# Kernel optimization log

Hardware: AMD Instinct MI355X
Metric: run time of the kernel (lower is better)

The kernel has to match this reference:

```python
import jax, jax.numpy as jnp
import numpy as np

D_MODEL = 1024
NUM_HEADS = 16
D_K = D_MODEL // NUM_HEADS
NEG = -1000000000.0


def setup_inputs() -> dict:
    key = jax.random.key(0)
    ks = jax.random.split(key, 9)
    B, S, D = 2, 2048, D_MODEL
    scale = 1.0 / np.sqrt(D)
    return {
        "query": jax.random.normal(ks[0], (B, S, D), jnp.float32),
        "key": jax.random.normal(ks[1], (B, S, D), jnp.float32),
        "value": jax.random.normal(ks[2], (B, S, D), jnp.float32),
        "mask": jax.random.randint(ks[3], (B, S, S), 0, 2, jnp.int32),
        # torch nn.Linear stores weight as (out_features, in_features); y = x @ W.T
        "W_q": jax.random.normal(ks[4], (D, D), jnp.float32) * scale,
        "W_k": jax.random.normal(ks[5], (D, D), jnp.float32) * scale,
        "W_v": jax.random.normal(ks[6], (D, D), jnp.float32) * scale,
        "W_o": jax.random.normal(ks[7], (D, D), jnp.float32) * scale,
        "b_o": jax.random.normal(ks[8], (D,), jnp.float32) * 0.01,
    }


def reference(query, key, value, mask, W_q, W_k, W_v, W_o, b_o):
    B, S, D = query.shape
    H, dk = NUM_HEADS, D_K
    # projections (torch Linear: x @ W.T), then split heads -> [B, H, S, dk]
    def split_heads(x, W):
        return jnp.einsum('bsd,ed->bse', x, W).reshape(B, S, H, dk).transpose(0, 2, 1, 3)
    Q = split_heads(query, W_q)
    K = split_heads(key, W_k)
    V = split_heads(value, W_v)
    scores = jnp.einsum('bhqd,bhkd->bhqk', Q, K) / jnp.sqrt(jnp.float32(dk))
    scores = jnp.where(mask[:, None, :, :] == 0, NEG, scores)
    attn = jax.nn.softmax(scores, axis=-1)  # dropout inactive in eval mode
    out = jnp.einsum('bhqk,bhkd->bhqd', attn, V)  # [B, H, S, dk]
    out = out.transpose(0, 2, 1, 3).reshape(B, S, D)
    return jnp.einsum('bsd,ed->bse', out, W_o) + b_o
```

## Files before the change

### kernel.cpp

```cpp
#include <hip/hip_runtime.h>
#include <hip/hip_bf16.h>
#include <stdint.h>

typedef __attribute__((ext_vector_type(4))) float f32x4;
typedef __attribute__((ext_vector_type(8))) short bf16x8;
typedef __attribute__((ext_vector_type(4))) unsigned short us4;
typedef unsigned short ushort_t;
typedef unsigned long long u64;

#define LOG2E 1.44269504088896340f
#define NEGB  -1.0e9f

__device__ __forceinline__ unsigned short f2bf(float x){
  union { float f; uint32_t u; } v; v.f = x;
  uint32_t u = v.u + 0x7fffu + ((v.u >> 16) & 1u);
  return (unsigned short)(u >> 16);
}

__device__ __forceinline__ void gld16(const void* g, void* l){
  __builtin_amdgcn_global_load_lds(
      (const __attribute__((address_space(1))) unsigned int*)g,
      (__attribute__((address_space(3))) unsigned int*)l, 16, 0, 0);
}

__global__ void prep_all(const float4* __restrict__ q, const float4* __restrict__ k,
                         const float4* __restrict__ v, const float4* __restrict__ wq,
                         const float4* __restrict__ wk, const float4* __restrict__ wv,
                         const float4* __restrict__ wo, ushort_t* __restrict__ dst,
                         const int4* __restrict__ mask, u64* __restrict__ mb){
  int bid = blockIdx.x;
  if (bid < 16384){
    int i = bid * 256 + threadIdx.x;
    const float4* src; int base;
    if      (i < 1048576){ src = q;  base = 0; }
    else if (i < 2097152){ src = k;  base = 1048576; }
    else if (i < 3145728){ src = v;  base = 2097152; }
    else if (i < 3407872){ src = wq; base = 3145728; }
    else if (i < 3670016){ src = wk; base = 3407872; }
    else if (i < 3932160){ src = wv; base = 3670016; }
    else                 { src = wo; base = 3932160; }
    float4 f = src[i - base];
    us4 o; o.x = f2bf(f.x); o.y = f2bf(f.y); o.z = f2bf(f.z); o.w = f2bf(f.w);
    ((us4*)dst)[i] = o;
  } else {
    int w = (bid - 16384) * 256 + threadIdx.x;
    const int4* p = mask + (size_t)w * 16;
    u64 bits = 0;
    #pragma unroll
    for (int j = 0; j < 16; j++){
      int4 m = p[j];
      bits |= (u64)(m.x != 0) << (j*4);
      bits |= (u64)(m.y != 0) << (j*4+1);
      bits |= (u64)(m.z != 0) << (j*4+2);
      bits |= (u64)(m.w != 0) << (j*4+3);
    }
    mb[w] = bits;
  }
}

__global__ void gemm_qkv(const ushort_t* __restrict__ qb, const ushort_t* __restrict__ kb,
                         const ushort_t* __restrict__ vb, const ushort_t* __restrict__ wqb,
                         const ushort_t* __restrict__ wkb, const ushort_t* __restrict__ wvb,
                         ushort_t* __restrict__ Qh, ushort_t* __restrict__ Kh,
                         ushort_t* __restrict__ Vt, float qscale){
  __shared__ ushort_t As[2][4096];
  __shared__ ushort_t Bs[2][4096];
  const int z = blockIdx.z;
  const ushort_t* A = (z == 0) ? qb  : (z == 1) ? kb  : vb;
  const ushort_t* B = (z == 0) ? wqb : (z == 1) ? wkb : wvb;
  ushort_t*       C = (z == 0) ? Qh  : (z == 1) ? Kh  : Vt;
  const float scale = (z == 0) ? qscale : 1.0f;

  const int tid = threadIdx.x, wave = tid >> 6, lane = tid & 63;
  const int m0 = blockIdx.x * 128, n0 = blockIdx.y * 128;
  const int wr = wave >> 1, wc = wave & 1;
  f32x4 acc[4][4] = {};

  const ushort_t* Ag = A + (size_t)(m0 + wave*16 + (lane>>2)) * 1024 + (lane&3)*8;
  const ushort_t* Bg = B + (size_t)(n0 + wave*16 + (lane>>2)) * 1024 + (lane&3)*8;

#define GSTAGE(k0, c) do { \
    gld16(Ag + (k0),         &As[c][wave*512]); \
    gld16(Ag + 65536 + (k0), &As[c][(4+wave)*512]); \
    gld16(Bg + (k0),         &Bs[c][wave*512]); \
    gld16(Bg + 65536 + (k0), &Bs[c][(4+wave)*512]); } while(0)

  GSTAGE(0, 0);
  int cur = 0;
  for (int k0 = 0; k0 < 1024; k0 += 32){
    __syncthreads();
    if (k0 < 992) GSTAGE(k0 + 32, cur ^ 1);
    bf16x8 a[4], b[4];
    #pragma unroll
    for (int i = 0; i < 4; i++){
      a[i] = *(const bf16x8*)&As[cur][(wr*64 + i*16 + (lane&15))*32 + (lane>>4)*8];
      b[i] = *(const bf16x8*)&Bs[cur][(wc*64 + i*16 + (lane&15))*32 + (lane>>4)*8];
    }
    __builtin_amdgcn_s_setprio(1);
    #pragma unroll
    for (int i = 0; i < 4; i++)
      #pragma unroll
      for (int j = 0; j < 4; j++)
        acc[i][j] = __builtin_amdgcn_mfma_f32_16x16x32_bf16(a[i], b[j], acc[i][j], 0, 0, 0);
    __builtin_amdgcn_s_setprio(0);
    cur ^= 1;
  }

  #pragma unroll
  for (int i = 0; i < 4; i++){
    #pragma unroll
    for (int j = 0; j < 4; j++){
      #pragma unroll
      for (int r = 0; r < 4; r++){
        int row = m0 + wr*64 + i*16 + (lane>>4)*4 + r;
        int col = n0 + wc*64 + j*16 + (lane&15);
        int bb = row >> 11, s = row & 2047, h = col >> 6, d = col & 63;
        unsigned short bv = f2bf(acc[i][j][r] * scale);
        if (z < 2) C[((size_t)(bb*16 + h)*2048 + s)*64 + d] = bv;
        else       C[((size_t)(bb*16 + h)*64 + d)*2048 + s] = bv;
      }
    }
  }
}

__global__ void gemm_out(const ushort_t* __restrict__ A, const ushort_t* __restrict__ B,
                         float* __restrict__ C, const float* __restrict__ bias){
  __shared__ ushort_t As[2][4096];
  __shared__ ushort_t Bs[2][4096];
  const int tid = threadIdx.x, wave = tid >> 6, lane = tid & 63;
  const int m0 = blockIdx.x * 128, n0 = blockIdx.y * 128;
  const int wr = wave >> 1, wc = wave & 1;
  f32x4 acc[4][4] = {};

  const ushort_t* Ag = A + (size_t)(m0 + wave*16 + (lane>>2)) * 1024 + (lane&3)*8;
  const ushort_t* Bg = B + (size_t)(n0 + wave*16 + (lane>>2)) * 1024 + (lane&3)*8;

  GSTAGE(0, 0);
  int cur = 0;
  for (int k0 = 0; k0 < 1024; k0 += 32){
    __syncthreads();
    if (k0 < 992) GSTAGE(k0 + 32, cur ^ 1);
    bf16x8 a[4], b[4];
    #pragma unroll
    for (int i = 0; i < 4; i++){
      a[i] = *(const bf16x8*)&As[cur][(wr*64 + i*16 + (lane&15))*32 + (lane>>4)*8];
      b[i] = *(const bf16x8*)&Bs[cur][(wc*64 + i*16 + (lane&15))*32 + (lane>>4)*8];
    }
    __builtin_amdgcn_s_setprio(1);
    #pragma unroll
    for (int i = 0; i < 4; i++)
      #pragma unroll
      for (int j = 0; j < 4; j++)
        acc[i][j] = __builtin_amdgcn_mfma_f32_16x16x32_bf16(a[i], b[j], acc[i][j], 0, 0, 0);
    __builtin_amdgcn_s_setprio(0);
    cur ^= 1;
  }

  #pragma unroll
  for (int i = 0; i < 4; i++){
    #pragma unroll
    for (int j = 0; j < 4; j++){
      #pragma unroll
      for (int r = 0; r < 4; r++){
        int row = m0 + wr*64 + i*16 + (lane>>4)*4 + r;
        int col = n0 + wc*64 + j*16 + (lane&15);
        C[(size_t)row * 1024 + col] = acc[i][j][r] + bias[col];
      }
    }
  }
}

__global__ void attn_fused(const ushort_t* __restrict__ Qh, const ushort_t* __restrict__ Kh,
                           const ushort_t* __restrict__ Vt, const u64* __restrict__ MB,
                           ushort_t* __restrict__ AO){
  __shared__ ushort_t Ks[2][4096];
  __shared__ ushort_t Vs[2][4096];
  __shared__ ushort_t Pb[4][1024];

  const int tid = threadIdx.x, wave = tid >> 6, lane = tid & 63;
  const int g = lane >> 4, l15 = lane & 15;
  const int wg = ((blockIdx.x & 7) << 7) | (blockIdx.x >> 3);
  const int qt = wg & 31, h = (wg >> 5) & 15, b = wg >> 9;
  const int q0 = qt * 64;

  const ushort_t* Qb = Qh + ((size_t)(b*16 + h)*2048 + q0) * 64;
  const ushort_t* Kb = Kh + ((size_t)(b*16 + h)*2048) * 64;
  const ushort_t* Vb = Vt + ((size_t)(b*16 + h)*64) * 2048;
  const u64* wp = MB + ((size_t)b*2048 + q0 + wave*16 + l15) * 32;

  bf16x8 qf[2];
  #pragma unroll
  for (int ks = 0; ks < 2; ks++)
    qf[ks] = *(const bf16x8*)&Qb[(wave*16 + l15)*64 + ks*32 + g*8];

  bf16x8 onesb;
  #pragma unroll
  for (int j = 0; j < 8; j++) onesb[j] = (short)0x3F80;

  f32x4 o[4] = {};
  f32x4 osum = {};

  const int srow = lane >> 3;
  const int scol = ((lane & 7) * 16) ^ (srow << 4);
  const ushort_t* Kg = Kb + (size_t)(wave*8 + srow)*64   + (scol >> 1);
  const ushort_t* Vg = Vb + (size_t)(wave*8 + srow)*2048 + (scol >> 1);
  ushort_t* pb = &Pb[wave][0];
  const int xv = (l15 & 7) << 4;
  const int g4 = g * 4;

#define ASTAGE(t, c) do { \
    gld16(Kg + (size_t)(t)*4096,         &Ks[c][wave*512]); \
    gld16(Kg + (size_t)(t)*4096 + 2048,  &Ks[c][(4+wave)*512]); \
    gld16(Vg + (t)*64,                   &Vs[c][wave*512]); \
    gld16(Vg + 65536 + (t)*64,           &Vs[c][(4+wave)*512]); } while(0)

  ASTAGE(0, 0);
  u64 w = wp[0];
  int cur = 0;

  for (int t = 0; t < 32; t++){
    __syncthreads();
    if (t < 31) ASTAGE(t + 1, cur ^ 1);
    u64 wnext = (t < 31) ? wp[t + 1] : 0;

    f32x4 sa[4] = {};
    __builtin_amdgcn_s_setprio(1);
    #pragma unroll
    for (int nf = 0; nf < 4; nf++){
      #pragma unroll
      for (int ks = 0; ks < 2; ks++){
        int row = nf*16 + l15;
        int cb  = (ks*64 + g*16) ^ ((row & 7) << 4);
        bf16x8 kf = *(const bf16x8*)&Ks[cur][row*64 + (cb >> 1)];
        sa[nf] = __builtin_amdgcn_mfma_f32_16x16x32_bf16(kf, qf[ks], sa[nf], 0, 0, 0);
      }
    }
    __builtin_amdgcn_s_setprio(0);

    uint32_t s0 = ((uint32_t)w) >> g4;
    uint32_t s1 = ((uint32_t)(w >> 32)) >> g4;
    float p[4][4];
    #pragma unroll
    for (int nf = 0; nf < 4; nf++){
      uint32_t ws = (nf < 2) ? s0 : s1;
      const int sh = (nf & 1) * 16;
      #pragma unroll
      for (int r = 0; r < 4; r++){
        float s = ((ws >> (sh + r)) & 1u) ? sa[nf][r] : NEGB;
        p[nf][r] = __builtin_amdgcn_exp2f(s);
      }
    }

    #pragma unroll
    for (int nf = 0; nf < 4; nf++){
      __hip_bfloat162 lo, hi;
      lo.x = __float2bfloat16(p[nf][0]); lo.y = __float2bfloat16(p[nf][1]);
      hi.x = __float2bfloat16(p[nf][2]); hi.y = __float2bfloat16(p[nf][3]);
      uint2 pk; pk.x = *(uint32_t*)&lo; pk.y = *(uint32_t*)&hi;
      int byte = l15*128 + ((nf*32 + g*8) ^ xv);
      *(uint2*)((char*)pb + byte) = pk;
    }
    asm volatile("s_waitcnt lgkmcnt(0)" ::: "memory");

    bf16x8 pa[2];
    #pragma unroll
    for (int c = 0; c < 2; c++){
      int cb = (c*64 + g*16) ^ xv;
      pa[c] = *(const bf16x8*)((const char*)pb + l15*128 + cb);
    }
    __builtin_amdgcn_s_setprio(1);
    #pragma unroll
    for (int df = 0; df < 4; df++){
      #pragma unroll
      for (int c = 0; c < 2; c++){
        int vrow = df*16 + l15;
        int cb = (c*64 + g*16) ^ ((vrow & 7) << 4);
        bf16x8 vf = *(const bf16x8*)&Vs[cur][vrow*64 + (cb >> 1)];
        o[df] = __builtin_amdgcn_mfma_f32_16x16x32_bf16(pa[c], vf, o[df], 0, 0, 0);
      }
    }
    osum = __builtin_amdgcn_mfma_f32_16x16x32_bf16(pa[0], onesb, osum, 0, 0, 0);
    osum = __builtin_amdgcn_mfma_f32_16x16x32_bf16(pa[1], onesb, osum, 0, 0, 0);
    __builtin_amdgcn_s_setprio(0);
    w = wnext;
    cur ^= 1;
  }

  float li[4];
  #pragma unroll
  for (int r = 0; r < 4; r++) li[r] = 1.0f / osum[r];
  #pragma unroll
  for (int df = 0; df < 4; df++){
    #pragma unroll
    for (int r = 0; r < 4; r++){
      int s = q0 + wave*16 + g4 + r;
      int d = h*64 + df*16 + l15;
      AO[((size_t)b*2048 + s)*1024 + d] = f2bf(o[df][r] * li[r]);
    }
  }
}

extern "C" void kernel_launch(void* const* d_in, const int* in_sizes, int n_in,
                              void* d_out, int out_size, void* d_ws, size_t ws_size,
                              hipStream_t stream){
  const float* q   = (const float*)d_in[0];
  const float* k   = (const float*)d_in[1];
  const float* v   = (const float*)d_in[2];
  const int*   msk = (const int*)  d_in[3];
  const float* wq  = (const float*)d_in[4];
  const float* wk  = (const float*)d_in[5];
  const float* wv  = (const float*)d_in[6];
  const float* wo  = (const float*)d_in[7];
  const float* bo  = (const float*)d_in[8];

  char* ws = (char*)d_ws;
  ushort_t* conv = (ushort_t*)ws;
  ushort_t* qb  = conv;
  ushort_t* kb  = conv + 4194304;
  ushort_t* vb  = conv + 8388608;
  ushort_t* wqb = conv + 12582912;
  ushort_t* wkb = conv + 13631488;
  ushort_t* wvb = conv + 14680064;
  ushort_t* wob = conv + 15728640;
  u64*      mbits = (u64*)(ws + 33554432);
  ushort_t* Qh  = (ushort_t*)(ws + 34603008);
  ushort_t* Kh  = (ushort_t*)(ws + 42991616);
  ushort_t* Vt  = kb;
  ushort_t* AO  = qb;

  prep_all<<<16896, 256, 0, stream>>>((const float4*)q, (const float4*)k,
      (const float4*)v, (const float4*)wq, (const float4*)wk, (const float4*)wv,
      (const float4*)wo, conv, (const int4*)msk, mbits);

  const float qscale = 0.125f * LOG2E;
  gemm_qkv<<<dim3(32, 8, 3), 256, 0, stream>>>(qb, kb, vb, wqb, wkb, wvb,
                                               Qh, Kh, Vt, qscale);

  attn_fused<<<1024, 256, 0, stream>>>(Qh, Kh, Vt, mbits, AO);

  gemm_out<<<dim3(32, 8), 256, 0, stream>>>(AO, wob, (float*)d_out, bo);
}
```

Measured before the change: 157.6 us.

## Enlarge attention tile to 128 queries with 8 waves; transpose V stores via LDS

```diff
diff --git a/kernel.cpp b/kernel.cpp
--- a/kernel.cpp
+++ b/kernel.cpp
@@ -63,8 +63,9 @@
                          const ushort_t* __restrict__ wkb, const ushort_t* __restrict__ wvb,
                          ushort_t* __restrict__ Qh, ushort_t* __restrict__ Kh,
                          ushort_t* __restrict__ Vt, float qscale){
-  __shared__ ushort_t As[2][4096];
-  __shared__ ushort_t Bs[2][4096];
+  __shared__ ushort_t smem[16384];
+#define AsQ(c) (smem + (c)*4096)
+#define BsQ(c) (smem + 8192 + (c)*4096)
   const int z = blockIdx.z;
   const ushort_t* A = (z == 0) ? qb  : (z == 1) ? kb  : vb;
   const ushort_t* B = (z == 0) ? wqb : (z == 1) ? wkb : wvb;
@@ -72,6 +73,7 @@
   const float scale = (z == 0) ? qscale : 1.0f;
 
   const int tid = threadIdx.x, wave = tid >> 6, lane = tid & 63;
+  const int l15 = lane & 15;
   const int m0 = blockIdx.x * 128, n0 = blockIdx.y * 128;
   const int wr = wave >> 1, wc = wave & 1;
   f32x4 acc[4][4] = {};
@@ -80,10 +82,10 @@
   const ushort_t* Bg = B + (size_t)(n0 + wave*16 + (lane>>2)) * 1024 + (lane&3)*8;
 
 #define GSTAGE(k0, c) do { \
-    gld16(Ag + (k0),         &As[c][wave*512]); \
-    gld16(Ag + 65536 + (k0), &As[c][(4+wave)*512]); \
-    gld16(Bg + (k0),         &Bs[c][wave*512]); \
-    gld16(Bg + 65536 + (k0), &Bs[c][(4+wave)*512]); } while(0)
+    gld16(Ag + (k0),         AsQ(c) + wave*512); \
+    gld16(Ag + 65536 + (k0), AsQ(c) + (4+wave)*512); \
+    gld16(Bg + (k0),         BsQ(c) + wave*512); \
+    gld16(Bg + 65536 + (k0), BsQ(c) + (4+wave)*512); } while(0)
 
   GSTAGE(0, 0);
   int cur = 0;
@@ -93,8 +95,8 @@
     bf16x8 a[4], b[4];
     #pragma unroll
     for (int i = 0; i < 4; i++){
-      a[i] = *(const bf16x8*)&As[cur][(wr*64 + i*16 + (lane&15))*32 + (lane>>4)*8];
-      b[i] = *(const bf16x8*)&Bs[cur][(wc*64 + i*16 + (lane&15))*32 + (lane>>4)*8];
+      a[i] = *(const bf16x8*)&AsQ(cur)[(wr*64 + i*16 + l15)*32 + (lane>>4)*8];
+      b[i] = *(const bf16x8*)&BsQ(cur)[(wc*64 + i*16 + l15)*32 + (lane>>4)*8];
     }
     __builtin_amdgcn_s_setprio(1);
     #pragma unroll
@@ -106,18 +108,50 @@
     cur ^= 1;
   }
 
-  #pragma unroll
-  for (int i = 0; i < 4; i++){
-    #pragma unroll
-    for (int j = 0; j < 4; j++){
-      #pragma unroll
-      for (int r = 0; r < 4; r++){
-        int row = m0 + wr*64 + i*16 + (lane>>4)*4 + r;
-        int col = n0 + wc*64 + j*16 + (lane&15);
-        int bb = row >> 11, s = row & 2047, h = col >> 6, d = col & 63;
-        unsigned short bv = f2bf(acc[i][j][r] * scale);
-        if (z < 2) C[((size_t)(bb*16 + h)*2048 + s)*64 + d] = bv;
-        else       C[((size_t)(bb*16 + h)*64 + d)*2048 + s] = bv;
+  if (z < 2){
+    #pragma unroll
+    for (int i = 0; i < 4; i++){
+      #pragma unroll
+      for (int j = 0; j < 4; j++){
+        #pragma unroll
+        for (int r = 0; r < 4; r++){
+          int row = m0 + wr*64 + i*16 + (lane>>4)*4 + r;
+          int col = n0 + wc*64 + j*16 + l15;
+          int bb = row >> 11, s = row & 2047, h = col >> 6, d = col & 63;
+          C[((size_t)(bb*16 + h)*2048 + s)*64 + d] = f2bf(acc[i][j][r] * scale);
+        }
+      }
+    }
+  } else {
+    ushort_t* T = smem;
+    #pragma unroll
+    for (int hh = 0; hh < 2; hh++){
+      __syncthreads();
+      if (wc == hh){
+        #pragma unroll
+        for (int i = 0; i < 4; i++){
+          #pragma unroll
+          for (int j = 0; j < 4; j++){
+            int n = j*16 + l15;
+            int mb2 = wr*64 + i*16 + (lane>>4)*4;
+            us4 pk;
+            pk.x = f2bf(acc[i][j][0]); pk.y = f2bf(acc[i][j][1]);
+            pk.z = f2bf(acc[i][j][2]); pk.w = f2bf(acc[i][j][3]);
+            *(us4*)&T[n*136 + mb2] = pk;
+          }
+        }
+      }
+      __syncthreads();
+      #pragma unroll
+      for (int cc = 0; cc < 4; cc++){
+        int chunk = cc*256 + tid;
+        int n = chunk >> 4, mc = chunk & 15;
+        uint4 val = *(uint4*)&T[n*136 + mc*8];
+        int col = n0 + hh*64 + n;
+        int hcol = col >> 6, d = col & 63;
+        int row = m0 + mc*8;
+        int bb2 = row >> 11, s = row & 2047;
+        *(uint4*)&C[((size_t)(bb2*16 + hcol)*64 + d)*2048 + s] = val;
       }
     }
   }
@@ -135,11 +169,17 @@
   const ushort_t* Ag = A + (size_t)(m0 + wave*16 + (lane>>2)) * 1024 + (lane&3)*8;
   const ushort_t* Bg = B + (size_t)(n0 + wave*16 + (lane>>2)) * 1024 + (lane&3)*8;
 
-  GSTAGE(0, 0);
+#define GSTAGE2(k0, c) do { \
+    gld16(Ag + (k0),         &As[c][wave*512]); \
+    gld16(Ag + 65536 + (k0), &As[c][(4+wave)*512]); \
+    gld16(Bg + (k0),         &Bs[c][wave*512]); \
+    gld16(Bg + 65536 + (k0), &Bs[c][(4+wave)*512]); } while(0)
+
+  GSTAGE2(0, 0);
   int cur = 0;
   for (int k0 = 0; k0 < 1024; k0 += 32){
     __syncthreads();
-    if (k0 < 992) GSTAGE(k0 + 32, cur ^ 1);
+    if (k0 < 992) GSTAGE2(k0 + 32, cur ^ 1);
     bf16x8 a[4], b[4];
     #pragma unroll
     for (int i = 0; i < 4; i++){
@@ -175,13 +215,13 @@
                            ushort_t* __restrict__ AO){
   __shared__ ushort_t Ks[2][4096];
   __shared__ ushort_t Vs[2][4096];
-  __shared__ ushort_t Pb[4][1024];
+  __shared__ ushort_t Pb[8][1024];
 
   const int tid = threadIdx.x, wave = tid >> 6, lane = tid & 63;
   const int g = lane >> 4, l15 = lane & 15;
-  const int wg = ((blockIdx.x & 7) << 7) | (blockIdx.x >> 3);
-  const int qt = wg & 31, h = (wg >> 5) & 15, b = wg >> 9;
-  const int q0 = qt * 64;
+  const int wg = ((blockIdx.x & 7) << 6) | (blockIdx.x >> 3);
+  const int qt = wg & 15, h = (wg >> 4) & 15, b = wg >> 8;
+  const int q0 = qt * 128;
 
   const ushort_t* Qb = Qh + ((size_t)(b*16 + h)*2048 + q0) * 64;
   const ushort_t* Kb = Kh + ((size_t)(b*16 + h)*2048) * 64;
@@ -209,10 +249,8 @@
   const int g4 = g * 4;
 
 #define ASTAGE(t, c) do { \
-    gld16(Kg + (size_t)(t)*4096,         &Ks[c][wave*512]); \
-    gld16(Kg + (size_t)(t)*4096 + 2048,  &Ks[c][(4+wave)*512]); \
-    gld16(Vg + (t)*64,                   &Vs[c][wave*512]); \
-    gld16(Vg + 65536 + (t)*64,           &Vs[c][(4+wave)*512]); } while(0)
+    gld16(Kg + (size_t)(t)*4096, &Ks[c][wave*512]); \
+    gld16(Vg + (t)*64,           &Vs[c][wave*512]); } while(0)
 
   ASTAGE(0, 0);
   u64 w = wp[0];
@@ -325,7 +363,7 @@
   u64*      mbits = (u64*)(ws + 33554432);
   ushort_t* Qh  = (ushort_t*)(ws + 34603008);
   ushort_t* Kh  = (ushort_t*)(ws + 42991616);
-  ushort_t* Vt  = kb;
+  ushort_t* Vt  = (ushort_t*)d_out;
   ushort_t* AO  = qb;
 
   prep_all<<<16896, 256, 0, stream>>>((const float4*)q, (const float4*)k,
@@ -336,7 +374,7 @@
   gemm_qkv<<<dim3(32, 8, 3), 256, 0, stream>>>(qb, kb, vb, wqb, wkb, wvb,
                                                Qh, Kh, Vt, qscale);
 
-  attn_fused<<<1024, 256, 0, stream>>>(Qh, Kh, Vt, mbits, AO);
+  attn_fused<<<512, 512, 0, stream>>>(Qh, Kh, Vt, mbits, AO);
 
   gemm_out<<<dim3(32, 8), 256, 0, stream>>>(AO, wob, (float*)d_out, bo);
 }
```

After: 150.2 us. 4.7% less time.
